# Kernel tuning notes

Measured on AMD Instinct MI355X. Metric: run time of the kernel, lower is better.

## Reference

```python
import jax, jax.numpy as jnp
import numpy as np

N_NODES = 50000
ALPHA = 0.1
K_ITERS = 10


def setup_inputs() -> dict:
    key = jax.random.key(0)
    ks = jax.random.split(key, 6)
    x = jax.random.normal(ks[0], (N_NODES, 256), dtype=jnp.float32)
    edge_index = jax.random.randint(ks[1], (2, 800000), 0, N_NODES, dtype=jnp.int64)
    # Glorot-ish scaled weights
    W1 = jax.random.normal(ks[2], (256, 128), dtype=jnp.float32) * (1.0 / np.sqrt(256))
    b1 = jnp.zeros((128,), dtype=jnp.float32)
    W3 = jax.random.normal(ks[3], (128, 64), dtype=jnp.float32) * (1.0 / np.sqrt(128))
    b3 = jnp.zeros((64,), dtype=jnp.float32)
    return {"x": x, "edge_index": edge_index, "W1": W1, "b1": b1, "W3": W3, "b3": b3}


def _gcn_norm(edge_index, n_nodes):
    # Add self-loops, then symmetric normalization D^{-1/2} (A+I) D^{-1/2}
    loops = jnp.arange(n_nodes, dtype=edge_index.dtype)
    src = jnp.concatenate([edge_index[0], loops])
    dst = jnp.concatenate([edge_index[1], loops])
    deg = jax.ops.segment_sum(jnp.ones_like(dst, dtype=jnp.float32), dst,
                              num_segments=n_nodes)
    dinv = jnp.where(deg > 0, jax.lax.rsqrt(deg), 0.0)
    w = dinv[src] * dinv[dst]  # [E + N]
    return src, dst, w


def _propagate(h, src, dst, w, n_nodes):
    # out[dst] += w * h[src]  (gather -> scale -> scatter-add)
    msgs = w[:, None] * h[src]
    return jax.ops.segment_sum(msgs, dst, num_segments=n_nodes)


def reference(x, edge_index, W1, b1, W3, b3):
    n = x.shape[0]
    src, dst, w = _gcn_norm(edge_index, n)

    # GCNConv 1: linear then normalized propagation
    h = _propagate(x @ W1 + b1, src, dst, w, n)

    # APPNP: K iterations of h = (1-alpha)*A_hat h + alpha*h0 (eval: no edge dropout)
    h0 = h

    def step(hc, _):
        hn = (1.0 - ALPHA) * _propagate(hc, src, dst, w, n) + ALPHA * h0
        return hn, None

    h, _ = jax.lax.scan(step, h, None, length=K_ITERS)

    # GCNConv 2
    out = _propagate(h @ W3 + b3, src, dst, w, n)
    return out
```

## Files before the change

### kernel.cpp

```cpp
#include <hip/hip_runtime.h>

#define NN 50000
#define NE 800000
#define NTP (NE + 8 * NN)


__global__ void zero_deg_kernel(int* deg) {
  int v = blockIdx.x * 256 + threadIdx.x;
  if (v < NN) deg[v] = 0;
}

__global__ void count_deg_kernel(const int* __restrict__ edst, int* __restrict__ deg) {
  int i = blockIdx.x * 256 + threadIdx.x;
  if (i < NE) atomicAdd(&deg[edst[i]], 1);
}

__global__ void dinv_kernel(const int* __restrict__ deg, float* __restrict__ dinv) {
  int v = blockIdx.x * 256 + threadIdx.x;
  if (v < NN) dinv[v] = rsqrtf((float)(deg[v] + 1));
}

__device__ __forceinline__ int pdeg_of(int deg) {
  return ((deg + 8) >> 3) << 3;
}

__global__ __launch_bounds__(1024) void scan1_kernel(const int* __restrict__ deg,
                                                     int* __restrict__ incl,
                                                     int* __restrict__ bsum) {
  __shared__ int sd[1024];
  int gid = blockIdx.x * 1024 + threadIdx.x;
  int v = (gid < NN) ? pdeg_of(deg[gid]) : 0;
  sd[threadIdx.x] = v;
  __syncthreads();
  for (int off = 1; off < 1024; off <<= 1) {
    int t = (threadIdx.x >= off) ? sd[threadIdx.x - off] : 0;
    __syncthreads();
    sd[threadIdx.x] += t;
    __syncthreads();
  }
  if (gid < NN) incl[gid] = sd[threadIdx.x];
  if (threadIdx.x == 1023) bsum[blockIdx.x] = sd[1023];
}

__global__ void scan2_kernel(int* bsum, int nb) {
  if (threadIdx.x == 0 && blockIdx.x == 0) {
    int run = 0;
    for (int i = 0; i < nb; ++i) { int t = bsum[i]; bsum[i] = run; run += t; }
  }
}

__global__ void scan3_kernel(const int* __restrict__ deg, const int* __restrict__ incl,
                             const int* __restrict__ bsum, int* __restrict__ offs,
                             int* __restrict__ cursor) {
  int v = blockIdx.x * 256 + threadIdx.x;
  if (v >= NN) return;
  int pd = pdeg_of(deg[v]);
  int o = bsum[v >> 10] + incl[v] - pd;
  offs[v] = o;
  cursor[v] = o;
  if (v == NN - 1) offs[NN] = o + pd;
}

__global__ void zero_edges_kernel(int2* edges) {
  int i = blockIdx.x * 256 + threadIdx.x;
  if (i < NTP) edges[i] = make_int2(0, 0);
}

__global__ void fill_kernel(const int* __restrict__ esrc, const int* __restrict__ edst,
                            const float* __restrict__ dinv, int* __restrict__ cursor,
                            int2* __restrict__ edges) {
  int i = blockIdx.x * 256 + threadIdx.x;
  if (i >= NE + NN) return;
  int s, d;
  if (i < NE) { s = esrc[i]; d = edst[i]; }
  else        { s = d = i - NE; }
  int p = atomicAdd(&cursor[d], 1);
  int2 e;
  e.x = s;
  e.y = __float_as_int(dinv[s] * dinv[d]);
  edges[p] = e;
}

__global__ void rowsum_kernel(const int* __restrict__ offs, const int2* __restrict__ edges,
                              float* __restrict__ rowsum) {
  int v = blockIdx.x * 256 + threadIdx.x;
  if (v >= NN) return;
  float s = 0.f;
  int e1 = offs[v + 1];
  for (int e = offs[v]; e < e1; ++e) s += __int_as_float(edges[e].y);
  rowsum[v] = s;
}


__global__ void w13_kernel(const float* __restrict__ W1, const float* __restrict__ W3,
                           float* __restrict__ W13) {
  int idx = blockIdx.x * 256 + threadIdx.x;
  if (idx >= 256 * 64) return;
  int r = idx >> 6, c = idx & 63;
  float acc = 0.f;
  for (int k = 0; k < 128; ++k) acc += W1[r * 128 + k] * W3[k * 64 + c];
  W13[idx] = acc;
}

__global__ void b13_kernel(const float* __restrict__ b1, const float* __restrict__ W3,
                           float* __restrict__ b13) {
  int c = threadIdx.x;
  if (c >= 64) return;
  float acc = 0.f;
  for (int k = 0; k < 128; ++k) acc += b1[k] * W3[k * 64 + c];
  b13[c] = acc;
}


template <int K>
__global__ __launch_bounds__(256) void gemm64_kernel(const float* __restrict__ A,
                                                     const float* __restrict__ W,
                                                     const float* __restrict__ bias,
                                                     float* __restrict__ out, int M) {
  __shared__ float xs[64][36];
  __shared__ float ws[32][64];

  int tid = threadIdx.x;
  int tc = tid & 15;
  int tr = tid >> 4;
  int row0 = blockIdx.x * 64;

  float acc[4][4] = {};

  for (int kc = 0; kc < K; kc += 32) {
    for (int i = tid; i < 512; i += 256) {
      int r = i >> 3, k4 = i & 7;
      int row = row0 + r;
      float4 v = make_float4(0.f, 0.f, 0.f, 0.f);
      if (row < M) v = *reinterpret_cast<const float4*>(&A[(size_t)row * K + kc + k4 * 4]);
      *reinterpret_cast<float4*>(&xs[r][k4 * 4]) = v;
    }
    for (int i = tid; i < 512; i += 256) {
      int k = i >> 4, c4 = i & 15;
      *reinterpret_cast<float4*>(&ws[k][c4 * 4]) =
          *reinterpret_cast<const float4*>(&W[(size_t)(kc + k) * 64 + c4 * 4]);
    }
    __syncthreads();
#pragma unroll
    for (int kk = 0; kk < 32; kk += 4) {
      float4 xv[4], wv[4];
#pragma unroll
      for (int r = 0; r < 4; ++r)
        xv[r] = *reinterpret_cast<const float4*>(&xs[tr * 4 + r][kk]);
#pragma unroll
      for (int q = 0; q < 4; ++q)
        wv[q] = *reinterpret_cast<const float4*>(&ws[kk + q][tc * 4]);
#pragma unroll
      for (int r = 0; r < 4; ++r) {
        acc[r][0] += xv[r].x * wv[0].x + xv[r].y * wv[1].x + xv[r].z * wv[2].x + xv[r].w * wv[3].x;
        acc[r][1] += xv[r].x * wv[0].y + xv[r].y * wv[1].y + xv[r].z * wv[2].y + xv[r].w * wv[3].y;
        acc[r][2] += xv[r].x * wv[0].z + xv[r].y * wv[1].z + xv[r].z * wv[2].z + xv[r].w * wv[3].z;
        acc[r][3] += xv[r].x * wv[0].w + xv[r].y * wv[1].w + xv[r].z * wv[2].w + xv[r].w * wv[3].w;
      }
    }
    __syncthreads();
  }

  float4 bv = *reinterpret_cast<const float4*>(&bias[tc * 4]);
#pragma unroll
  for (int r = 0; r < 4; ++r) {
    int row = row0 + tr * 4 + r;
    if (row < M) {
      float4 o;
      o.x = acc[r][0] + bv.x;
      o.y = acc[r][1] + bv.y;
      o.z = acc[r][2] + bv.z;
      o.w = acc[r][3] + bv.w;
      *reinterpret_cast<float4*>(&out[(size_t)row * 64 + tc * 4]) = o;
    }
  }
}


template <int MODE>
__global__ __launch_bounds__(256) void prop64_kernel(const float* __restrict__ hin,
                                                     const float* __restrict__ h0,
                                                     float* __restrict__ out,
                                                     const int* __restrict__ offs,
                                                     const int2* __restrict__ edges,
                                                     const float* __restrict__ rowsum,
                                                     const float* __restrict__ b3) {
  int node = blockIdx.x * 16 + (threadIdx.x >> 4);
  if (node >= NN) return;
  int f = (threadIdx.x & 15) * 4;
  const float* __restrict__ hb = hin + f;

  int e = offs[node];
  int e1 = offs[node + 1];
  float ax = 0.f, ay = 0.f, az = 0.f, aw = 0.f;

  for (; e < e1; e += 8) {
    int4 m01 = *reinterpret_cast<const int4*>(edges + e);
    int4 m23 = *reinterpret_cast<const int4*>(edges + e + 2);
    int4 m45 = *reinterpret_cast<const int4*>(edges + e + 4);
    int4 m67 = *reinterpret_cast<const int4*>(edges + e + 6);
    float4 v0 = *reinterpret_cast<const float4*>(hb + (size_t)m01.x * 64);
    float4 v1 = *reinterpret_cast<const float4*>(hb + (size_t)m01.z * 64);
    float4 v2 = *reinterpret_cast<const float4*>(hb + (size_t)m23.x * 64);
    float4 v3 = *reinterpret_cast<const float4*>(hb + (size_t)m23.z * 64);
    float4 v4 = *reinterpret_cast<const float4*>(hb + (size_t)m45.x * 64);
    float4 v5 = *reinterpret_cast<const float4*>(hb + (size_t)m45.z * 64);
    float4 v6 = *reinterpret_cast<const float4*>(hb + (size_t)m67.x * 64);
    float4 v7 = *reinterpret_cast<const float4*>(hb + (size_t)m67.z * 64);
    float w0 = __int_as_float(m01.y), w1 = __int_as_float(m01.w);
    float w2 = __int_as_float(m23.y), w3 = __int_as_float(m23.w);
    float w4 = __int_as_float(m45.y), w5 = __int_as_float(m45.w);
    float w6 = __int_as_float(m67.y), w7 = __int_as_float(m67.w);
    ax += w0 * v0.x + w1 * v1.x + w2 * v2.x + w3 * v3.x
        + w4 * v4.x + w5 * v5.x + w6 * v6.x + w7 * v7.x;
    ay += w0 * v0.y + w1 * v1.y + w2 * v2.y + w3 * v3.y
        + w4 * v4.y + w5 * v5.y + w6 * v6.y + w7 * v7.y;
    az += w0 * v0.z + w1 * v1.z + w2 * v2.z + w3 * v3.z
        + w4 * v4.z + w5 * v5.z + w6 * v6.z + w7 * v7.z;
    aw += w0 * v0.w + w1 * v1.w + w2 * v2.w + w3 * v3.w
        + w4 * v4.w + w5 * v5.w + w6 * v6.w + w7 * v7.w;
  }

  if (MODE == 1) {
    float4 z = *reinterpret_cast<const float4*>(&h0[(size_t)node * 64 + f]);
    ax = 0.9f * ax + 0.1f * z.x;
    ay = 0.9f * ay + 0.1f * z.y;
    az = 0.9f * az + 0.1f * z.z;
    aw = 0.9f * aw + 0.1f * z.w;
  }
  if (MODE == 2) {
    float rs = rowsum[node];
    float4 bz = *reinterpret_cast<const float4*>(&b3[f]);
    ax += rs * bz.x; ay += rs * bz.y; az += rs * bz.z; aw += rs * bz.w;
  }
  float4 o = make_float4(ax, ay, az, aw);
  *reinterpret_cast<float4*>(&out[(size_t)node * 64 + f]) = o;
}


extern "C" void kernel_launch(void* const* d_in, const int* in_sizes, int n_in,
                              void* d_out, int out_size, void* d_ws, size_t ws_size,
                              hipStream_t stream) {
  const float* x    = (const float*)d_in[0];
  const int*   eidx = (const int*)d_in[1];
  const float* W1   = (const float*)d_in[2];
  const float* b1   = (const float*)d_in[3];
  const float* W3   = (const float*)d_in[4];
  const float* b3   = (const float*)d_in[5];
  float* outp = (float*)d_out;

  const int* esrc = eidx;
  const int* edst = eidx + NE;

  char* w = (char*)d_ws;
  size_t off = 0;
  auto take = [&](size_t bytes) {
    void* p = w + off;
    off = (off + bytes + 255) & ~(size_t)255;
    return p;
  };
  int*   deg    = (int*)take(NN * 4);
  float* dinv   = (float*)take(NN * 4);
  int*   incl   = (int*)take(NN * 4);
  int*   offs   = (int*)take((NN + 1) * 4);
  int*   cursor = (int*)take(NN * 4);
  int*   bsum   = (int*)take(64 * 4);
  float* rsum   = (float*)take(NN * 4);
  float* W13    = (float*)take(256 * 64 * 4);
  float* b13    = (float*)take(64 * 4);
  int2*  edges  = (int2*)take((size_t)NTP * 8);
  float* y0     = (float*)take((size_t)NN * 64 * 4);
  float* z0     = (float*)take((size_t)NN * 64 * 4);
  float* zp     = (float*)take((size_t)NN * 64 * 4);
  float* zq     = (float*)take((size_t)NN * 64 * 4);
  (void)ws_size; (void)in_sizes; (void)n_in; (void)out_size;

  const int nblkN = (NN + 255) / 256;
  const int nblkE = (NE + 255) / 256;
  const int nblkF = (NE + NN + 255) / 256;
  const int nblkP = (NTP + 255) / 256;
  const int nbScan = (NN + 1023) / 1024;

  w13_kernel<<<64, 256, 0, stream>>>(W1, W3, W13);
  b13_kernel<<<1, 64, 0, stream>>>(b1, W3, b13);

  zero_deg_kernel<<<nblkN, 256, 0, stream>>>(deg);
  count_deg_kernel<<<nblkE, 256, 0, stream>>>(edst, deg);
  dinv_kernel<<<nblkN, 256, 0, stream>>>(deg, dinv);
  scan1_kernel<<<nbScan, 1024, 0, stream>>>(deg, incl, bsum);
  scan2_kernel<<<1, 64, 0, stream>>>(bsum, nbScan);
  scan3_kernel<<<nblkN, 256, 0, stream>>>(deg, incl, bsum, offs, cursor);
  zero_edges_kernel<<<nblkP, 256, 0, stream>>>(edges);
  fill_kernel<<<nblkF, 256, 0, stream>>>(esrc, edst, dinv, cursor, edges);
  rowsum_kernel<<<nblkN, 256, 0, stream>>>(offs, edges, rsum);

  gemm64_kernel<256><<<(NN + 63) / 64, 256, 0, stream>>>(x, W13, b13, y0, NN);

  const int pblk = (NN + 15) / 16;

  prop64_kernel<0><<<pblk, 256, 0, stream>>>(y0, nullptr, z0, offs, edges, nullptr, nullptr);

  const float* hc = z0;
  float* bufs[2] = {zp, zq};
  for (int it = 0; it < 10; ++it) {
    float* hn = bufs[it & 1];
    prop64_kernel<1><<<pblk, 256, 0, stream>>>(hc, z0, hn, offs, edges, nullptr, nullptr);
    hc = hn;
  }

  prop64_kernel<2><<<pblk, 256, 0, stream>>>(hc, nullptr, outp, offs, edges, rsum, b3);
}
```

Baseline: 512.8 us.

## Double-buffer GEMM shared tiles and make fill kernel grid-stride

The 64-column GEMM now keeps two shared-memory buffers and prefetches the next K-chunk into registers while computing on the current one, so each chunk needs one barrier instead of two. This is meant to hide global load latency behind the FMA loop, at the cost of twice the LDS and extra registers per thread. Separately, the CSR fill kernel becomes a grid-stride loop over 832 blocks instead of one thread per edge, which cuts block count but serializes several atomics per thread.

```diff
diff --git a/kernel.cpp b/kernel.cpp
--- a/kernel.cpp
+++ b/kernel.cpp
@@ -66,19 +66,21 @@
   if (i < NTP) edges[i] = make_int2(0, 0);
 }
 
+#define FILL_STRIDE (832 * 256)
 __global__ void fill_kernel(const int* __restrict__ esrc, const int* __restrict__ edst,
                             const float* __restrict__ dinv, int* __restrict__ cursor,
                             int2* __restrict__ edges) {
   int i = blockIdx.x * 256 + threadIdx.x;
-  if (i >= NE + NN) return;
-  int s, d;
-  if (i < NE) { s = esrc[i]; d = edst[i]; }
-  else        { s = d = i - NE; }
-  int p = atomicAdd(&cursor[d], 1);
-  int2 e;
-  e.x = s;
-  e.y = __float_as_int(dinv[s] * dinv[d]);
-  edges[p] = e;
+  for (; i < NE + NN; i += FILL_STRIDE) {
+    int s, d;
+    if (i < NE) { s = esrc[i]; d = edst[i]; }
+    else        { s = d = i - NE; }
+    int p = atomicAdd(&cursor[d], 1);
+    int2 e;
+    e.x = s;
+    e.y = __float_as_int(dinv[s] * dinv[d]);
+    edges[p] = e;
+  }
 }
 
 __global__ void rowsum_kernel(const int* __restrict__ offs, const int2* __restrict__ edges,
@@ -117,39 +119,54 @@
                                                      const float* __restrict__ W,
                                                      const float* __restrict__ bias,
                                                      float* __restrict__ out, int M) {
-  __shared__ float xs[64][36];
-  __shared__ float ws[32][64];
+  __shared__ float xs[2][64][36];
+  __shared__ float ws[2][32][64];
 
   int tid = threadIdx.x;
   int tc = tid & 15;
   int tr = tid >> 4;
   int row0 = blockIdx.x * 64;
 
+  int xr = tid >> 3, xk = (tid & 7) * 4;
+  int wk = tid >> 4, wc = (tid & 15) * 4;
+
+  float4 ax0, ax1, aw0, aw1;
+  const float4 z4 = make_float4(0.f, 0.f, 0.f, 0.f);
+
+  auto loadchunk = [&](int kc) {
+    int row = row0 + xr;
+    ax0 = (row < M) ? *reinterpret_cast<const float4*>(&A[(size_t)row * K + kc + xk]) : z4;
+    row = row0 + xr + 32;
+    ax1 = (row < M) ? *reinterpret_cast<const float4*>(&A[(size_t)row * K + kc + xk]) : z4;
+    aw0 = *reinterpret_cast<const float4*>(&W[(size_t)(kc + wk) * 64 + wc]);
+    aw1 = *reinterpret_cast<const float4*>(&W[(size_t)(kc + wk + 16) * 64 + wc]);
+  };
+  auto storechunk = [&](int b) {
+    *reinterpret_cast<float4*>(&xs[b][xr][xk]) = ax0;
+    *reinterpret_cast<float4*>(&xs[b][xr + 32][xk]) = ax1;
+    *reinterpret_cast<float4*>(&ws[b][wk][wc]) = aw0;
+    *reinterpret_cast<float4*>(&ws[b][wk + 16][wc]) = aw1;
+  };
+
   float acc[4][4] = {};
-
-  for (int kc = 0; kc < K; kc += 32) {
-    for (int i = tid; i < 512; i += 256) {
-      int r = i >> 3, k4 = i & 7;
-      int row = row0 + r;
-      float4 v = make_float4(0.f, 0.f, 0.f, 0.f);
-      if (row < M) v = *reinterpret_cast<const float4*>(&A[(size_t)row * K + kc + k4 * 4]);
-      *reinterpret_cast<float4*>(&xs[r][k4 * 4]) = v;
-    }
-    for (int i = tid; i < 512; i += 256) {
-      int k = i >> 4, c4 = i & 15;
-      *reinterpret_cast<float4*>(&ws[k][c4 * 4]) =
-          *reinterpret_cast<const float4*>(&W[(size_t)(kc + k) * 64 + c4 * 4]);
-    }
-    __syncthreads();
+  constexpr int NCH = K / 32;
+
+  loadchunk(0);
+  storechunk(0);
+  __syncthreads();
+
+  for (int t = 0; t < NCH; ++t) {
+    int cur = t & 1;
+    if (t + 1 < NCH) loadchunk((t + 1) * 32);
 #pragma unroll
     for (int kk = 0; kk < 32; kk += 4) {
       float4 xv[4], wv[4];
 #pragma unroll
       for (int r = 0; r < 4; ++r)
-        xv[r] = *reinterpret_cast<const float4*>(&xs[tr * 4 + r][kk]);
+        xv[r] = *reinterpret_cast<const float4*>(&xs[cur][tr * 4 + r][kk]);
 #pragma unroll
       for (int q = 0; q < 4; ++q)
-        wv[q] = *reinterpret_cast<const float4*>(&ws[kk + q][tc * 4]);
+        wv[q] = *reinterpret_cast<const float4*>(&ws[cur][kk + q][tc * 4]);
 #pragma unroll
       for (int r = 0; r < 4; ++r) {
         acc[r][0] += xv[r].x * wv[0].x + xv[r].y * wv[1].x + xv[r].z * wv[2].x + xv[r].w * wv[3].x;
@@ -158,6 +175,7 @@
         acc[r][3] += xv[r].x * wv[0].w + xv[r].y * wv[1].w + xv[r].z * wv[2].w + xv[r].w * wv[3].w;
       }
     }
+    if (t + 1 < NCH) storechunk(cur ^ 1);
     __syncthreads();
   }
 
@@ -277,7 +295,6 @@
 
   const int nblkN = (NN + 255) / 256;
   const int nblkE = (NE + 255) / 256;
-  const int nblkF = (NE + NN + 255) / 256;
   const int nblkP = (NTP + 255) / 256;
   const int nbScan = (NN + 1023) / 1024;
 
@@ -291,7 +308,7 @@
   scan2_kernel<<<1, 64, 0, stream>>>(bsum, nbScan);
   scan3_kernel<<<nblkN, 256, 0, stream>>>(deg, incl, bsum, offs, cursor);
   zero_edges_kernel<<<nblkP, 256, 0, stream>>>(edges);
-  fill_kernel<<<nblkF, 256, 0, stream>>>(esrc, edst, dinv, cursor, edges);
+  fill_kernel<<<832, 256, 0, stream>>>(esrc, edst, dinv, cursor, edges);
   rowsum_kernel<<<nblkN, 256, 0, stream>>>(offs, edges, rsum);
 
   gemm64_kernel<256><<<(NN + 63) / 64, 256, 0, stream>>>(x, W13, b13, y0, NN);
```

Result: slower. 523.0 us (+2.0%).
